# Performance work log

Measured on AMD Instinct MI355X. Metric: run time of the kernel, lower is better.

The kernel has to match this reference:

```python
import jax, jax.numpy as jnp
import numpy as np
from math import sqrt

B, S, E, H = 4, 2048, 1024, 16
D = E // H  # per-head dim = 64


def setup_inputs() -> dict:
    key = jax.random.key(0)
    ks = jax.random.split(key, 11)
    f = lambda k, shape, scale=1.0: jax.random.normal(k, shape, dtype=jnp.float32) * scale
    return {
        "Q": f(ks[0], (B, S, E)),
        "K": f(ks[1], (B, S, E)),
        "V": f(ks[2], (B, S, E)),
        "Wq": f(ks[3], (E, E), 1.0 / sqrt(E)),
        "bq": f(ks[4], (E,), 0.02),
        "Wk": f(ks[5], (E, E), 1.0 / sqrt(E)),
        "bk": f(ks[6], (E,), 0.02),
        "Wv": f(ks[7], (E, E), 1.0 / sqrt(E)),
        "bv": f(ks[8], (E,), 0.02),
        "Wo": f(ks[9], (E, E), 1.0 / sqrt(E)),
        "bo": f(ks[10], (E,), 0.02),
    }


def reference(Q, K, V, Wq, bq, Wk, bk, Wv, bv, Wo, bo):
    # Linear projections (torch Linear: x @ W.T + b)
    q = Q @ Wq.T + bq  # [B,S,E]
    k = K @ Wk.T + bk
    v = V @ Wv.T + bv
    # torch.chunk along last dim into H heads == reshape [B,S,H,D]
    q = q.reshape(B, S, H, D)
    k = k.reshape(B, S, H, D)
    v = v.reshape(B, S, H, D)
    scale = 1.0 / sqrt(D)
    # batched-over-heads scaled dot-product attention
    scores = jnp.einsum("bqhd,bkhd->bhqk", q, k) * scale  # [B,H,S,S]
    attn = jax.nn.softmax(scores, axis=-1)
    out = jnp.einsum("bhqk,bkhd->bqhd", attn, v).reshape(B, S, E)
    # dropout p=0.0 -> identity
    return out @ Wo.T + bo
```

## Files before the change

kernel.cpp:

```cpp
#include <hip/hip_runtime.h>
#include <hip/hip_bf16.h>

#define B_SZ   4
#define S_LEN  2048
#define E_DIM  1024
#define H_NUM  16
#define D_DIM  64
#define M_ROWS (B_SZ * S_LEN)
#define QK_SCALE 0.1803368801111204f

typedef __attribute__((ext_vector_type(8))) __bf16 bf16x8;
typedef __attribute__((ext_vector_type(4))) float  f32x4;

__device__ __forceinline__ bf16x8 load8(const void* p) {
    return __builtin_bit_cast(bf16x8, *reinterpret_cast<const uint4*>(p));
}

#if defined(__has_builtin)
#if __has_builtin(__builtin_amdgcn_exp2f)
#define EXP2F(x) __builtin_amdgcn_exp2f(x)
#endif
#if __has_builtin(__builtin_amdgcn_global_load_lds)
#define HAVE_GLL 1
#endif
#endif
#ifndef EXP2F
#define EXP2F(x) exp2f(x)
#endif

__device__ __forceinline__ void stage16(const __hip_bfloat16* g, __hip_bfloat16* lbase, int lane) {
#ifdef HAVE_GLL
    __builtin_amdgcn_global_load_lds((const __attribute__((address_space(1))) unsigned int*)g,
                                     (__attribute__((address_space(3))) unsigned int*)lbase,
                                     16, 0, 0);
#else
    reinterpret_cast<uint4*>(lbase)[lane] = *reinterpret_cast<const uint4*>(g);
#endif
}

#define N8A (1 << 20)
#define N8W (1 << 17)
#define N8TOT (3 * N8A + 4 * N8W)

struct CvtArgs {
    const float* s[7];
    __hip_bfloat16* d[7];
};

__global__ __launch_bounds__(256) void cvt_all(CvtArgs a)
{
    const int i = blockIdx.x * 256 + threadIdx.x;
    if (i >= N8TOT) return;
    int seg, off;
    if (i < 3 * N8A) { seg = i >> 20;              off = i & (N8A - 1); }
    else             { const int j = i - 3 * N8A;
                       seg = 3 + (j >> 17);        off = j & (N8W - 1); }
    const float* s = a.s[seg];
    __hip_bfloat16* d = a.d[seg];
    const float4 x = reinterpret_cast<const float4*>(s)[off * 2];
    const float4 y = reinterpret_cast<const float4*>(s)[off * 2 + 1];
    __hip_bfloat16 o[8];
    o[0] = __float2bfloat16(x.x); o[1] = __float2bfloat16(x.y);
    o[2] = __float2bfloat16(x.z); o[3] = __float2bfloat16(x.w);
    o[4] = __float2bfloat16(y.x); o[5] = __float2bfloat16(y.y);
    o[6] = __float2bfloat16(y.z); o[7] = __float2bfloat16(y.w);
    reinterpret_cast<uint4*>(d)[off] = *reinterpret_cast<uint4*>(o);
}

__global__ __launch_bounds__(256) void cvt_f32_bf16(const float* __restrict__ s,
                                                    __hip_bfloat16* __restrict__ d,
                                                    int n8)
{
    const int i = blockIdx.x * 256 + threadIdx.x;
    if (i >= n8) return;
    const float4 a = reinterpret_cast<const float4*>(s)[i * 2];
    const float4 b = reinterpret_cast<const float4*>(s)[i * 2 + 1];
    __hip_bfloat16 o[8];
    o[0] = __float2bfloat16(a.x); o[1] = __float2bfloat16(a.y);
    o[2] = __float2bfloat16(a.z); o[3] = __float2bfloat16(a.w);
    o[4] = __float2bfloat16(b.x); o[5] = __float2bfloat16(b.y);
    o[6] = __float2bfloat16(b.z); o[7] = __float2bfloat16(b.w);
    reinterpret_cast<uint4*>(d)[i] = *reinterpret_cast<uint4*>(o);
}

struct GemmArgs {
    const __hip_bfloat16* A[3];
    const __hip_bfloat16* W[3];
    const float* bias[3];
    void* C[3];
    float scale[3];
    int mode[3];
};

__global__ __launch_bounds__(512, 4) void gemm_bt(GemmArgs g)
{
    __shared__ __attribute__((aligned(16))) char lds_raw[3 * 24576];

    const int tid = threadIdx.x;
    const int wid = tid >> 6, lane = tid & 63;
    const int quad = lane >> 4, l16 = lane & 15;
    const int wm = wid >> 2, wn = wid & 3;

    const int seg = blockIdx.x >> 8;
    int bid = blockIdx.x & 255;
    bid = (bid & 7) * 32 + (bid >> 3);
    const int bm = bid >> 2, bn = bid & 3;
    const int row0 = bm * 128, col0 = bn * 256;

    const __hip_bfloat16* A = g.A[seg];
    const __hip_bfloat16* W = g.W[seg];

    const int s_line = tid >> 3, s_gr = tid & 7;
    const int glin  = s_gr ^ (s_line & 7);
    const int s_row = (s_line << 1) + (glin >> 2);
    const int s_ks  = glin & 3;
    const __hip_bfloat16* gA = A + (size_t)(row0 + s_row) * E_DIM + s_ks * 8;
    const __hip_bfloat16* gB = W + (size_t)(col0 + s_row) * E_DIM + s_ks * 8;
    const int stA = wid << 10;

    const int rg   = (((l16 & 1) << 2) | quad) ^ ((l16 >> 1) & 7);
    const int aoff = (wm * 32 + (l16 >> 1)) * 128 + rg * 16;
    const int boff = (wn * 32 + (l16 >> 1)) * 128 + rg * 16;

    f32x4 acc[4][4];
    const f32x4 zero = {0.f, 0.f, 0.f, 0.f};
#pragma unroll
    for (int i = 0; i < 4; i++)
#pragma unroll
        for (int j = 0; j < 4; j++) acc[i][j] = zero;

    auto stage_t = [&](int t) {
        char* b = lds_raw + (t % 3) * 24576;
        const int ko = t * 32;
        stage16(gA + ko, (__hip_bfloat16*)(b + stA), lane);
        stage16(gB + ko, (__hip_bfloat16*)(b + 8192 + stA), lane);
        stage16(gB + (size_t)128 * E_DIM + ko, (__hip_bfloat16*)(b + 16384 + stA), lane);
    };

    auto body = [&](int t, bool stg) {
        __builtin_amdgcn_s_barrier();
        __builtin_amdgcn_sched_barrier(0);
        if (stg) stage_t(t + 2);
        const char* ab = lds_raw + (t % 3) * 24576;
        bf16x8 af[4], bf[4];
#pragma unroll
        for (int i = 0; i < 4; i++) af[i] = load8(ab + aoff + i * 1024);
#pragma unroll
        for (int j = 0; j < 4; j++) bf[j] = load8(ab + 8192 + boff + j * 1024);
        __builtin_amdgcn_s_setprio(1);
#pragma unroll
        for (int i = 0; i < 4; i++)
#pragma unroll
            for (int j = 0; j < 4; j++)
                acc[i][j] = __builtin_amdgcn_mfma_f32_16x16x32_bf16(af[i], bf[j], acc[i][j], 0, 0, 0);
        __builtin_amdgcn_s_setprio(0);
        __builtin_amdgcn_sched_barrier(0);
    };

    const int NT = E_DIM / 32;
    stage_t(0); stage_t(1);
    for (int t = 0; t < NT - 2; ++t) {
        asm volatile("s_waitcnt vmcnt(3)" ::: "memory");
        body(t, true);
    }
    asm volatile("s_waitcnt vmcnt(3)" ::: "memory"); body(NT - 2, false);
    asm volatile("s_waitcnt vmcnt(0)" ::: "memory"); body(NT - 1, false);

    const int   mode  = g.mode[seg];
    const float scale = g.scale[seg];
    const float* bias = g.bias[seg];
    void* Cout        = g.C[seg];
#pragma unroll
    for (int j = 0; j < 4; j++) {
        const int col = col0 + wn * 64 + j * 16 + l16;
        const float bv = bias[col];
#pragma unroll
        for (int i = 0; i < 4; i++) {
            const int row = row0 + wm * 64 + i * 16 + quad * 4;
            if (mode == 3) {
                __attribute__((aligned(8))) __hip_bfloat16 o[4];
#pragma unroll
                for (int r = 0; r < 4; r++) o[r] = __float2bfloat16((acc[i][j][r] + bv) * scale);
                const int b_ = row >> 11, s_ = row & 2047, h_ = col >> 6, d_ = col & 63;
                *reinterpret_cast<uint2*>((__hip_bfloat16*)Cout +
                    (((size_t)(b_ * H_NUM + h_)) << 17) + (d_ << 11) + s_) =
                    *reinterpret_cast<uint2*>(o);
            } else {
#pragma unroll
                for (int r = 0; r < 4; r++) {
                    const float v = (acc[i][j][r] + bv) * scale;
                    const int rr = row + r;
                    if (mode == 0) {
                        ((__hip_bfloat16*)Cout)[(size_t)rr * E_DIM + col] = __float2bfloat16(v);
                    } else if (mode == 1) {
                        ((float*)Cout)[(size_t)rr * E_DIM + col] = v;
                    } else {
                        const int b_ = rr >> 11, s_ = rr & 2047, h_ = col >> 6, d_ = col & 63;
                        ((__hip_bfloat16*)Cout)[(((size_t)(b_ * H_NUM + h_)) << 17) + (s_ << 6) + d_] =
                            __float2bfloat16(v);
                    }
                }
            }
        }
    }
}

__global__ __launch_bounds__(256) void attn(const __hip_bfloat16* __restrict__ Qt,
                                            const __hip_bfloat16* __restrict__ Kt,
                                            const __hip_bfloat16* __restrict__ Vt,
                                            __hip_bfloat16* __restrict__ Op)
{
    __shared__ __hip_bfloat16 Pls[4][64][40];
    __shared__ __attribute__((aligned(16))) __hip_bfloat16 Kls[2][32 * 64];
    __shared__ __attribute__((aligned(16))) __hip_bfloat16 Vls[2][64 * 32];

    const int x = blockIdx.x;
    const int xcd = x & 7, idx = x >> 3;
    const int bh     = xcd * 8 + (idx & 7);
    const int qchunk = idx >> 3;
    const int tid = threadIdx.x;
    const int wave = tid >> 6, lane = tid & 63;
    const int quad = lane >> 4, l16 = lane & 15;
    const int qrow0 = qchunk * 256 + wave * 64;

    const __hip_bfloat16* qb = Qt + ((size_t)bh << 17);
    const __hip_bfloat16* kb = Kt + ((size_t)bh << 17);
    const __hip_bfloat16* vb = Vt + ((size_t)bh << 17);
    __hip_bfloat16* pw = &Pls[wave][0][0];

    const int skey = tid >> 3, sgk = (tid & 7) ^ (skey & 7);
    const __hip_bfloat16* kSrc = kb + (skey << 6) + (sgk << 3);
    const int sd = tid >> 2, sgv = (tid & 3) ^ ((sd >> 1) & 3);
    const __hip_bfloat16* vSrc = vb + ((size_t)sd << 11) + (sgv << 3);
    const int stW = wave << 10;

    const int ksw = l16 & 7, vsw = (l16 >> 1) & 3;

    bf16x8 qf[4][2];
#pragma unroll
    for (int qt = 0; qt < 4; qt++) {
        qf[qt][0] = load8(qb + ((qrow0 + qt * 16 + l16) << 6) + quad * 8);
        qf[qt][1] = load8(qb + ((qrow0 + qt * 16 + l16) << 6) + 32 + quad * 8);
    }

    const f32x4 zero = {0.f, 0.f, 0.f, 0.f};
    f32x4 o_acc[4][4];
#pragma unroll
    for (int qt = 0; qt < 4; qt++)
#pragma unroll
        for (int dj = 0; dj < 4; dj++) o_acc[qt][dj] = zero;
    float lsum[4] = {0.f, 0.f, 0.f, 0.f};

    auto stageKV = [&](int kv, int b) {
        stage16(kSrc + (kv << 6), (__hip_bfloat16*)((char*)&Kls[b][0] + stW), lane);
        stage16(vSrc + kv,        (__hip_bfloat16*)((char*)&Vls[b][0] + stW), lane);
    };

    auto compute = [&](int b) {
        const char* Kbuf = (const char*)&Kls[b][0];
        const char* Vbuf = (const char*)&Vls[b][0];
#pragma unroll
        for (int t = 0; t < 2; t++) {
            const bf16x8 ka = load8(Kbuf + ((t * 16 + l16) << 7) + ((quad ^ ksw) << 4));
            const bf16x8 kc = load8(Kbuf + ((t * 16 + l16) << 7) + (((quad + 4) ^ ksw) << 4));
#pragma unroll
            for (int qt = 0; qt < 4; qt++) {
                f32x4 st = __builtin_amdgcn_mfma_f32_16x16x32_bf16(ka, qf[qt][0], zero, 0, 0, 0);
                st       = __builtin_amdgcn_mfma_f32_16x16x32_bf16(kc, qf[qt][1], st, 0, 0, 0);
                const float p0 = EXP2F(st[0]), p1 = EXP2F(st[1]);
                const float p2 = EXP2F(st[2]), p3 = EXP2F(st[3]);
                lsum[qt] += (p0 + p1) + (p2 + p3);
                const unsigned u0 = (unsigned)__bfloat16_as_ushort(__float2bfloat16(p0));
                const unsigned u1 = (unsigned)__bfloat16_as_ushort(__float2bfloat16(p1));
                const unsigned u2 = (unsigned)__bfloat16_as_ushort(__float2bfloat16(p2));
                const unsigned u3 = (unsigned)__bfloat16_as_ushort(__float2bfloat16(p3));
                uint2 w;
                w.x = (u1 << 16) | u0;
                w.y = (u3 << 16) | u2;
                *reinterpret_cast<uint2*>(&pw[(qt * 16 + l16) * 40 + t * 16 + quad * 4]) = w;
            }
        }
        bf16x8 vf[4];
#pragma unroll
        for (int dj = 0; dj < 4; dj++)
            vf[dj] = load8(Vbuf + ((dj * 16 + l16) << 6) + ((quad ^ vsw) << 4));
        __builtin_amdgcn_s_setprio(1);
#pragma unroll
        for (int qt = 0; qt < 4; qt++) {
            const bf16x8 pa = load8(&pw[(qt * 16 + l16) * 40 + quad * 8]);
#pragma unroll
            for (int dj = 0; dj < 4; dj++)
                o_acc[qt][dj] = __builtin_amdgcn_mfma_f32_16x16x32_bf16(pa, vf[dj], o_acc[qt][dj], 0, 0, 0);
        }
        __builtin_amdgcn_s_setprio(0);
    };

    stageKV(0, 0);
    int cur = 0;
    for (int kv0 = 0; kv0 < S_LEN; kv0 += 32) {
        __syncthreads();
        if (kv0 + 32 < S_LEN) stageKV(kv0 + 32, cur ^ 1);
        compute(cur);
        cur ^= 1;
    }

    const int b_ = bh >> 4, h_ = bh & 15;
#pragma unroll
    for (int qt = 0; qt < 4; qt++) {
        float l = lsum[qt];
        l += __shfl_xor(l, 16, 64);
        l += __shfl_xor(l, 32, 64);
#pragma unroll
        for (int r = 0; r < 4; r++) {
            const float lr = __shfl(l, quad * 4 + r, 64);
            const float inv = 1.f / lr;
            const size_t ro = ((size_t)b_ * S_LEN + (qrow0 + qt * 16 + quad * 4 + r)) * E_DIM + h_ * D_DIM;
#pragma unroll
            for (int dj = 0; dj < 4; dj++)
                Op[ro + dj * 16 + l16] = __float2bfloat16(o_acc[qt][dj][r] * inv);
        }
    }
}

extern "C" void kernel_launch(void* const* d_in, const int* in_sizes, int n_in,
                              void* d_out, int out_size, void* d_ws, size_t ws_size,
                              hipStream_t stream)
{
    const float* Qf  = (const float*)d_in[0];
    const float* Kf  = (const float*)d_in[1];
    const float* Vf  = (const float*)d_in[2];
    const float* Wqf = (const float*)d_in[3];
    const float* bqf = (const float*)d_in[4];
    const float* Wkf = (const float*)d_in[5];
    const float* bkf = (const float*)d_in[6];
    const float* Wvf = (const float*)d_in[7];
    const float* bvf = (const float*)d_in[8];
    const float* Wof = (const float*)d_in[9];
    const float* bof = (const float*)d_in[10];

    const size_t n_act = (size_t)M_ROWS * E_DIM;
    const size_t n_w   = (size_t)E_DIM * E_DIM;

    const dim3 blk(256), gblk(512), ablk(256);
    const int cg_act = (int)(n_act / 8 / 256);
    const int cg_w   = (int)(n_w / 8 / 256);

    const size_t need_fast = (6 * n_act + 4 * n_w) * sizeof(__hip_bfloat16);

    if (ws_size >= need_fast) {
        __hip_bfloat16* Xq = (__hip_bfloat16*)d_ws;
        __hip_bfloat16* Xk = Xq + n_act;
        __hip_bfloat16* Xv = Xk + n_act;
        __hip_bfloat16* Wb = Xv + n_act;
        __hip_bfloat16* Qt = Wb + 4 * n_w;
        __hip_bfloat16* Kt = Qt + n_act;
        __hip_bfloat16* Vt = Kt + n_act;

        CvtArgs ca;
        ca.s[0] = Qf;  ca.s[1] = Kf;  ca.s[2] = Vf;
        ca.s[3] = Wqf; ca.s[4] = Wkf; ca.s[5] = Wvf; ca.s[6] = Wof;
        ca.d[0] = Xq;  ca.d[1] = Xk;  ca.d[2] = Xv;
        ca.d[3] = Wb;  ca.d[4] = Wb + n_w; ca.d[5] = Wb + 2 * n_w; ca.d[6] = Wb + 3 * n_w;
        cvt_all<<<dim3(N8TOT / 256), blk, 0, stream>>>(ca);

        GemmArgs qkv;
        qkv.A[0] = Xq;  qkv.A[1] = Xk;  qkv.A[2] = Xv;
        qkv.W[0] = Wb;  qkv.W[1] = Wb + n_w;  qkv.W[2] = Wb + 2*n_w;
        qkv.bias[0] = bqf;  qkv.bias[1] = bkf;  qkv.bias[2] = bvf;
        qkv.C[0] = Qt;  qkv.C[1] = Kt;  qkv.C[2] = Vt;
        qkv.scale[0] = QK_SCALE;  qkv.scale[1] = 1.0f;  qkv.scale[2] = 1.0f;
        qkv.mode[0] = 2;  qkv.mode[1] = 2;  qkv.mode[2] = 3;
        gemm_bt<<<dim3(768), gblk, 0, stream>>>(qkv);

        attn<<<dim3(512), ablk, 0, stream>>>(Qt, Kt, Vt, Xq);

        GemmArgs og;
        og.A[0] = Xq;  og.A[1] = Xq;  og.A[2] = Xq;
        og.W[0] = Wb + 3*n_w;  og.W[1] = og.W[0];  og.W[2] = og.W[0];
        og.bias[0] = bof;  og.bias[1] = bof;  og.bias[2] = bof;
        og.C[0] = d_out;  og.C[1] = d_out;  og.C[2] = d_out;
        og.scale[0] = 1.0f;  og.scale[1] = 1.0f;  og.scale[2] = 1.0f;
        og.mode[0] = 1;  og.mode[1] = 1;  og.mode[2] = 1;
        gemm_bt<<<dim3(256), gblk, 0, stream>>>(og);
    } else {
        __hip_bfloat16* X  = (__hip_bfloat16*)d_ws;
        __hip_bfloat16* Wb = X + n_act;
        __hip_bfloat16* Qt = Wb + n_w;
        __hip_bfloat16* Kt = Qt + n_act;
        __hip_bfloat16* Vt = Kt + n_act;

        auto one = [&](const float* Af, const float* Wf, const float* bf_,
                       void* C, float sc, int md) {
            cvt_f32_bf16<<<cg_act, blk, 0, stream>>>(Af, X, (int)(n_act / 8));
            cvt_f32_bf16<<<cg_w,   blk, 0, stream>>>(Wf, Wb, (int)(n_w / 8));
            GemmArgs a;
            a.A[0] = X; a.A[1] = X; a.A[2] = X;
            a.W[0] = Wb; a.W[1] = Wb; a.W[2] = Wb;
            a.bias[0] = bf_; a.bias[1] = bf_; a.bias[2] = bf_;
            a.C[0] = C; a.C[1] = C; a.C[2] = C;
            a.scale[0] = sc; a.scale[1] = sc; a.scale[2] = sc;
            a.mode[0] = md; a.mode[1] = md; a.mode[2] = md;
            gemm_bt<<<dim3(256), gblk, 0, stream>>>(a);
        };
        one(Qf, Wqf, bqf, Qt, QK_SCALE, 2);
        one(Kf, Wkf, bkf, Kt, 1.0f, 2);
        one(Vf, Wvf, bvf, Vt, 1.0f, 3);
        attn<<<dim3(512), ablk, 0, stream>>>(Qt, Kt, Vt, X);
        cvt_f32_bf16<<<cg_w, blk, 0, stream>>>(Wof, Wb, (int)(n_w / 8));
        GemmArgs og;
        og.A[0] = X; og.A[1] = X; og.A[2] = X;
        og.W[0] = Wb; og.W[1] = Wb; og.W[2] = Wb;
        og.bias[0] = bof; og.bias[1] = bof; og.bias[2] = bof;
        og.C[0] = d_out; og.C[1] = d_out; og.C[2] = d_out;
        og.scale[0] = 1.0f; og.scale[1] = 1.0f; og.scale[2] = 1.0f;
        og.mode[0] = 1; og.mode[1] = 1; og.mode[2] = 1;
        gemm_bt<<<dim3(256), gblk, 0, stream>>>(og);
    }
}
```

Measured before the change: 331.4 us.

## Enlarge GEMM tile to 256x256 with 4-phase pipeline; double attention block size

The projection GEMM moves from 128x256 tiles with K-step 32 and triple buffering to 256x256 tiles with K-step 64. Each iteration is split into four MFMA phases interleaved with staging of the next tile into a double-buffered 128KB LDS. This raises arithmetic intensity per byte loaded, at the cost of occupancy (launch bounds 2), far fewer blocks (384 and 128), and more accumulator registers. The attention kernel now uses 512 threads covering 512 query rows per block, with K and V staged by separate halves of the block, so each staged K/V tile is shared by more queries.

```diff
diff --git a/kernel.cpp b/kernel.cpp
--- a/kernel.cpp
+++ b/kernel.cpp
@@ -90,81 +90,120 @@
     void* C[3];
     float scale[3];
     int mode[3];
+    int nper;
 };
 
-__global__ __launch_bounds__(512, 4) void gemm_bt(GemmArgs g)
+__global__ __launch_bounds__(512, 2) void gemm_bt(GemmArgs g)
 {
-    __shared__ __attribute__((aligned(16))) char lds_raw[3 * 24576];
+    __shared__ __attribute__((aligned(16))) char lds[2][65536];
 
     const int tid = threadIdx.x;
     const int wid = tid >> 6, lane = tid & 63;
     const int quad = lane >> 4, l16 = lane & 15;
     const int wm = wid >> 2, wn = wid & 3;
 
-    const int seg = blockIdx.x >> 8;
-    int bid = blockIdx.x & 255;
-    bid = (bid & 7) * 32 + (bid >> 3);
+    const int cpx = gridDim.x >> 3;
+    const int id  = (blockIdx.x & 7) * cpx + (blockIdx.x >> 3);
+    const int seg = id / g.nper;
+    const int bid = id % g.nper;
     const int bm = bid >> 2, bn = bid & 3;
-    const int row0 = bm * 128, col0 = bn * 256;
+    const int row0 = bm * 256, col0 = bn * 256;
 
     const __hip_bfloat16* A = g.A[seg];
     const __hip_bfloat16* W = g.W[seg];
 
-    const int s_line = tid >> 3, s_gr = tid & 7;
-    const int glin  = s_gr ^ (s_line & 7);
-    const int s_row = (s_line << 1) + (glin >> 2);
-    const int s_ks  = glin & 3;
-    const __hip_bfloat16* gA = A + (size_t)(row0 + s_row) * E_DIM + s_ks * 8;
-    const __hip_bfloat16* gB = W + (size_t)(col0 + s_row) * E_DIM + s_ks * 8;
-    const int stA = wid << 10;
-
-    const int rg   = (((l16 & 1) << 2) | quad) ^ ((l16 >> 1) & 7);
-    const int aoff = (wm * 32 + (l16 >> 1)) * 128 + rg * 16;
-    const int boff = (wn * 32 + (l16 >> 1)) * 128 + rg * 16;
-
-    f32x4 acc[4][4];
+    const int srow = tid >> 3;
+    const int sgk  = (tid & 7) ^ (srow & 7);
+    const __hip_bfloat16* aSrc = A + (size_t)(row0 + srow) * E_DIM + sgk * 8;
+    const __hip_bfloat16* bSrc = W + (size_t)(col0 + srow) * E_DIM + sgk * 8;
+    const int stW = wid << 10;
+
+    const int abase = (wm * 128 + l16) * 128;
+    const int bbase = 32768 + (wn * 64 + l16) * 128;
+    const int sl0 = ((quad)     ^ (l16 & 7)) << 4;
+    const int sl1 = ((quad | 4) ^ (l16 & 7)) << 4;
+
+    f32x4 acc[8][4];
     const f32x4 zero = {0.f, 0.f, 0.f, 0.f};
 #pragma unroll
-    for (int i = 0; i < 4; i++)
+    for (int i = 0; i < 8; i++)
 #pragma unroll
         for (int j = 0; j < 4; j++) acc[i][j] = zero;
 
-    auto stage_t = [&](int t) {
-        char* b = lds_raw + (t % 3) * 24576;
-        const int ko = t * 32;
-        stage16(gA + ko, (__hip_bfloat16*)(b + stA), lane);
-        stage16(gB + ko, (__hip_bfloat16*)(b + 8192 + stA), lane);
-        stage16(gB + (size_t)128 * E_DIM + ko, (__hip_bfloat16*)(b + 16384 + stA), lane);
+    auto stage = [&](int t, int c) {
+        char* d = lds[t & 1];
+        stage16(aSrc + (size_t)c * 64 * E_DIM + t * 64,
+                (__hip_bfloat16*)(d + c * 8192 + stW), lane);
+        stage16(bSrc + (size_t)c * 64 * E_DIM + t * 64,
+                (__hip_bfloat16*)(d + 32768 + c * 8192 + stW), lane);
     };
 
-    auto body = [&](int t, bool stg) {
+#define PHASE_TAIL()                                             \
+    __builtin_amdgcn_s_barrier();                                \
+    asm volatile("s_waitcnt lgkmcnt(0)" ::: "memory");           \
+    __builtin_amdgcn_sched_barrier(0);                           \
+    __builtin_amdgcn_s_setprio(1);
+
+#define PHASE_END()                                              \
+    __builtin_amdgcn_s_setprio(0);                               \
+    __builtin_amdgcn_s_barrier();
+
+    const int NT = E_DIM / 64;
+    stage(0, 0); stage(0, 1); stage(0, 2); stage(0, 3);
+    for (int t = 0; t < NT; ++t) {
+        const bool pf = (t + 1 < NT);
+        const char* base = lds[t & 1];
+        if (pf) { stage(t + 1, 0); stage(t + 1, 1);
+                  asm volatile("s_waitcnt vmcnt(4)" ::: "memory"); }
+        else    { asm volatile("s_waitcnt vmcnt(0)" ::: "memory"); }
         __builtin_amdgcn_s_barrier();
-        __builtin_amdgcn_sched_barrier(0);
-        if (stg) stage_t(t + 2);
-        const char* ab = lds_raw + (t % 3) * 24576;
+
         bf16x8 af[4], bf[4];
 #pragma unroll
-        for (int i = 0; i < 4; i++) af[i] = load8(ab + aoff + i * 1024);
-#pragma unroll
-        for (int j = 0; j < 4; j++) bf[j] = load8(ab + 8192 + boff + j * 1024);
-        __builtin_amdgcn_s_setprio(1);
+        for (int j = 0; j < 4; j++) bf[j] = load8(base + bbase + j * 2048 + sl0);
+#pragma unroll
+        for (int i = 0; i < 4; i++) af[i] = load8(base + abase + i * 2048 + sl0);
+        PHASE_TAIL()
 #pragma unroll
         for (int i = 0; i < 4; i++)
 #pragma unroll
             for (int j = 0; j < 4; j++)
                 acc[i][j] = __builtin_amdgcn_mfma_f32_16x16x32_bf16(af[i], bf[j], acc[i][j], 0, 0, 0);
-        __builtin_amdgcn_s_setprio(0);
-        __builtin_amdgcn_sched_barrier(0);
-    };
-
-    const int NT = E_DIM / 32;
-    stage_t(0); stage_t(1);
-    for (int t = 0; t < NT - 2; ++t) {
-        asm volatile("s_waitcnt vmcnt(3)" ::: "memory");
-        body(t, true);
-    }
-    asm volatile("s_waitcnt vmcnt(3)" ::: "memory"); body(NT - 2, false);
-    asm volatile("s_waitcnt vmcnt(0)" ::: "memory"); body(NT - 1, false);
+        PHASE_END()
+#pragma unroll
+        for (int i = 0; i < 4; i++) af[i] = load8(base + abase + (i + 4) * 2048 + sl0);
+        if (pf) stage(t + 1, 2);
+        PHASE_TAIL()
+#pragma unroll
+        for (int i = 0; i < 4; i++)
+#pragma unroll
+            for (int j = 0; j < 4; j++)
+                acc[i + 4][j] = __builtin_amdgcn_mfma_f32_16x16x32_bf16(af[i], bf[j], acc[i + 4][j], 0, 0, 0);
+        PHASE_END()
+#pragma unroll
+        for (int j = 0; j < 4; j++) bf[j] = load8(base + bbase + j * 2048 + sl1);
+#pragma unroll
+        for (int i = 0; i < 4; i++) af[i] = load8(base + abase + i * 2048 + sl1);
+        if (pf) stage(t + 1, 3);
+        PHASE_TAIL()
+#pragma unroll
+        for (int i = 0; i < 4; i++)
+#pragma unroll
+            for (int j = 0; j < 4; j++)
+                acc[i][j] = __builtin_amdgcn_mfma_f32_16x16x32_bf16(af[i], bf[j], acc[i][j], 0, 0, 0);
+        PHASE_END()
+#pragma unroll
+        for (int i = 0; i < 4; i++) af[i] = load8(base + abase + (i + 4) * 2048 + sl1);
+        PHASE_TAIL()
+#pragma unroll
+        for (int i = 0; i < 4; i++)
+#pragma unroll
+            for (int j = 0; j < 4; j++)
+                acc[i + 4][j] = __builtin_amdgcn_mfma_f32_16x16x32_bf16(af[i], bf[j], acc[i + 4][j], 0, 0, 0);
+        PHASE_END()
+    }
+#undef PHASE_TAIL
+#undef PHASE_END
 
     const int   mode  = g.mode[seg];
     const float scale = g.scale[seg];
@@ -175,8 +214,8 @@
         const int col = col0 + wn * 64 + j * 16 + l16;
         const float bv = bias[col];
 #pragma unroll
-        for (int i = 0; i < 4; i++) {
-            const int row = row0 + wm * 64 + i * 16 + quad * 4;
+        for (int i = 0; i < 8; i++) {
+            const int row = row0 + wm * 128 + i * 16 + quad * 4;
             if (mode == 3) {
                 __attribute__((aligned(8))) __hip_bfloat16 o[4];
 #pragma unroll
@@ -205,34 +244,34 @@
     }
 }
 
-__global__ __launch_bounds__(256) void attn(const __hip_bfloat16* __restrict__ Qt,
+__global__ __launch_bounds__(512) void attn(const __hip_bfloat16* __restrict__ Qt,
                                             const __hip_bfloat16* __restrict__ Kt,
                                             const __hip_bfloat16* __restrict__ Vt,
                                             __hip_bfloat16* __restrict__ Op)
 {
-    __shared__ __hip_bfloat16 Pls[4][64][40];
+    __shared__ __hip_bfloat16 Pls[8][64][40];
     __shared__ __attribute__((aligned(16))) __hip_bfloat16 Kls[2][32 * 64];
     __shared__ __attribute__((aligned(16))) __hip_bfloat16 Vls[2][64 * 32];
 
     const int x = blockIdx.x;
-    const int xcd = x & 7, idx = x >> 3;
-    const int bh     = xcd * 8 + (idx & 7);
-    const int qchunk = idx >> 3;
+    const int bh     = (x & 7) * 8 + ((x >> 3) & 7);
+    const int qchunk = x >> 6;
     const int tid = threadIdx.x;
     const int wave = tid >> 6, lane = tid & 63;
     const int quad = lane >> 4, l16 = lane & 15;
-    const int qrow0 = qchunk * 256 + wave * 64;
+    const int qrow0 = qchunk * 512 + wave * 64;
 
     const __hip_bfloat16* qb = Qt + ((size_t)bh << 17);
     const __hip_bfloat16* kb = Kt + ((size_t)bh << 17);
     const __hip_bfloat16* vb = Vt + ((size_t)bh << 17);
     __hip_bfloat16* pw = &Pls[wave][0][0];
 
-    const int skey = tid >> 3, sgk = (tid & 7) ^ (skey & 7);
+    const int rt = tid & 255;
+    const int skey = rt >> 3, sgk = (rt & 7) ^ (skey & 7);
     const __hip_bfloat16* kSrc = kb + (skey << 6) + (sgk << 3);
-    const int sd = tid >> 2, sgv = (tid & 3) ^ ((sd >> 1) & 3);
+    const int sd = rt >> 2, sgv = (rt & 3) ^ ((sd >> 1) & 3);
     const __hip_bfloat16* vSrc = vb + ((size_t)sd << 11) + (sgv << 3);
-    const int stW = wave << 10;
+    const int stW = (wave & 3) << 10;
 
     const int ksw = l16 & 7, vsw = (l16 >> 1) & 3;
 
@@ -252,8 +291,10 @@
     float lsum[4] = {0.f, 0.f, 0.f, 0.f};
 
     auto stageKV = [&](int kv, int b) {
-        stage16(kSrc + (kv << 6), (__hip_bfloat16*)((char*)&Kls[b][0] + stW), lane);
-        stage16(vSrc + kv,        (__hip_bfloat16*)((char*)&Vls[b][0] + stW), lane);
+        if (tid < 256)
+            stage16(kSrc + (kv << 6), (__hip_bfloat16*)((char*)&Kls[b][0] + stW), lane);
+        else
+            stage16(vSrc + kv,        (__hip_bfloat16*)((char*)&Vls[b][0] + stW), lane);
     };
 
     auto compute = [&](int b) {
@@ -341,7 +382,7 @@
     const size_t n_act = (size_t)M_ROWS * E_DIM;
     const size_t n_w   = (size_t)E_DIM * E_DIM;
 
-    const dim3 blk(256), gblk(512), ablk(256);
+    const dim3 blk(256), gblk(512), ablk(512);
     const int cg_act = (int)(n_act / 8 / 256);
     const int cg_w   = (int)(n_w / 8 / 256);
 
@@ -370,9 +411,10 @@
         qkv.C[0] = Qt;  qkv.C[1] = Kt;  qkv.C[2] = Vt;
         qkv.scale[0] = QK_SCALE;  qkv.scale[1] = 1.0f;  qkv.scale[2] = 1.0f;
         qkv.mode[0] = 2;  qkv.mode[1] = 2;  qkv.mode[2] = 3;
-        gemm_bt<<<dim3(768), gblk, 0, stream>>>(qkv);
-
-        attn<<<dim3(512), ablk, 0, stream>>>(Qt, Kt, Vt, Xq);
+        qkv.nper = 128;
+        gemm_bt<<<dim3(384), gblk, 0, stream>>>(qkv);
+
+        attn<<<dim3(256), ablk, 0, stream>>>(Qt, Kt, Vt, Xq);
 
         GemmArgs og;
         og.A[0] = Xq;  og.A[1] = Xq;  og.A[2] = Xq;
@@ -381,7 +423,8 @@
         og.C[0] = d_out;  og.C[1] = d_out;  og.C[2] = d_out;
         og.scale[0] = 1.0f;  og.scale[1] = 1.0f;  og.scale[2] = 1.0f;
         og.mode[0] = 1;  og.mode[1] = 1;  og.mode[2] = 1;
-        gemm_bt<<<dim3(256), gblk, 0, stream>>>(og);
+        og.nper = 128;
+        gemm_bt<<<dim3(128), gblk, 0, stream>>>(og);
     } else {
         __hip_bfloat16* X  = (__hip_bfloat16*)d_ws;
         __hip_bfloat16* Wb = X + n_act;
@@ -400,12 +443,13 @@
             a.C[0] = C; a.C[1] = C; a.C[2] = C;
             a.scale[0] = sc; a.scale[1] = sc; a.scale[2] = sc;
             a.mode[0] = md; a.mode[1] = md; a.mode[2] = md;
-            gemm_bt<<<dim3(256), gblk, 0, stream>>>(a);
+            a.nper = 128;
+            gemm_bt<<<dim3(128), gblk, 0, stream>>>(a);
         };
         one(Qf, Wqf, bqf, Qt, QK_SCALE, 2);
         one(Kf, Wkf, bkf, Kt, 1.0f, 2);
         one(Vf, Wvf, bvf, Vt, 1.0f, 3);
-        attn<<<dim3(512), ablk, 0, stream>>>(Qt, Kt, Vt, X);
+        attn<<<dim3(256), ablk, 0, stream>>>(Qt, Kt, Vt, X);
         cvt_f32_bf16<<<cg_w, blk, 0, stream>>>(Wof, Wb, (int)(n_w / 8));
         GemmArgs og;
         og.A[0] = X; og.A[1] = X; og.A[2] = X;
@@ -414,6 +458,7 @@
         og.C[0] = d_out; og.C[1] = d_out; og.C[2] = d_out;
         og.scale[0] = 1.0f; og.scale[1] = 1.0f; og.scale[2] = 1.0f;
         og.mode[0] = 1; og.mode[1] = 1; og.mode[2] = 1;
-        gemm_bt<<<dim3(256), gblk, 0, stream>>>(og);
-    }
-}
+        og.nper = 128;
+        gemm_bt<<<dim3(128), gblk, 0, stream>>>(og);
+    }
+}
```

Result: slower. 370.1 us (+11.7%).

## Fuse fp32-to-bf16 activation conversion into QKV projection GEMM

Applied to the files above, without the earlier changes.

Removes the separate conversion pass over the Q, K and V activations. The QKV GEMM now loads fp32 A tiles directly, converts them to bf16 in registers and writes them to LDS, while weights are still pre-converted by a smaller kernel. This avoids writing and rereading the bf16 activation copies, but A staging now goes through registers instead of direct global-to-LDS loads, which can add latency and register pressure in the main loop.

```diff
diff --git a/kernel.cpp b/kernel.cpp
--- a/kernel.cpp
+++ b/kernel.cpp
@@ -40,21 +40,17 @@
 
 #define N8A (1 << 20)
 #define N8W (1 << 17)
-#define N8TOT (3 * N8A + 4 * N8W)
-
-struct CvtArgs {
-    const float* s[7];
-    __hip_bfloat16* d[7];
+
+struct CvtWArgs {
+    const float* s[4];
+    __hip_bfloat16* d[4];
 };
 
-__global__ __launch_bounds__(256) void cvt_all(CvtArgs a)
+__global__ __launch_bounds__(256) void cvt_w(CvtWArgs a)
 {
     const int i = blockIdx.x * 256 + threadIdx.x;
-    if (i >= N8TOT) return;
-    int seg, off;
-    if (i < 3 * N8A) { seg = i >> 20;              off = i & (N8A - 1); }
-    else             { const int j = i - 3 * N8A;
-                       seg = 3 + (j >> 17);        off = j & (N8W - 1); }
+    if (i >= 4 * N8W) return;
+    const int seg = i >> 17, off = i & (N8W - 1);
     const float* s = a.s[seg];
     __hip_bfloat16* d = a.d[seg];
     const float4 x = reinterpret_cast<const float4*>(s)[off * 2];
@@ -92,7 +88,152 @@
     int mode[3];
 };
 
-__global__ __launch_bounds__(512, 4) void gemm_bt(GemmArgs g)
+struct GemmQArgs {
+    const float* Af[3];
+    const __hip_bfloat16* W[3];
+    const float* bias[3];
+    void* C[3];
+    float scale[3];
+    int mode[3];
+};
+
+__global__ __launch_bounds__(512, 4) void gemm_qkvf(GemmQArgs g)
+{
+    __shared__ __attribute__((aligned(16))) char lds_raw[3 * 24576];
+
+    const int tid = threadIdx.x;
+    const int wid = tid >> 6, lane = tid & 63;
+    const int quad = lane >> 4, l16 = lane & 15;
+    const int wm = wid >> 2, wn = wid & 3;
+
+    const int seg = blockIdx.x >> 8;
+    int bid = blockIdx.x & 255;
+    bid = (bid & 7) * 32 + (bid >> 3);
+    const int bm = bid >> 2, bn = bid & 3;
+    const int row0 = bm * 128, col0 = bn * 256;
+
+    const float* Af = g.Af[seg];
+    const __hip_bfloat16* W = g.W[seg];
+
+    const int s_line = tid >> 3, s_gr = tid & 7;
+    const int glin  = s_gr ^ (s_line & 7);
+    const int s_row = (s_line << 1) + (glin >> 2);
+    const int s_ks  = glin & 3;
+    const float* gAf = Af + (size_t)(row0 + s_row) * E_DIM + s_ks * 8;
+    const __hip_bfloat16* gB = W + (size_t)(col0 + s_row) * E_DIM + s_ks * 8;
+    const int stA = wid << 10;
+
+    const int rg   = (((l16 & 1) << 2) | quad) ^ ((l16 >> 1) & 7);
+    const int aoff = (wm * 32 + (l16 >> 1)) * 128 + rg * 16;
+    const int boff = (wn * 32 + (l16 >> 1)) * 128 + rg * 16;
+
+    f32x4 acc[4][4];
+    const f32x4 zero = {0.f, 0.f, 0.f, 0.f};
+#pragma unroll
+    for (int i = 0; i < 4; i++)
+#pragma unroll
+        for (int j = 0; j < 4; j++) acc[i][j] = zero;
+
+    auto stageB = [&](int t) {
+        char* b = lds_raw + (t % 3) * 24576;
+        const int ko = t * 32;
+        stage16(gB + ko, (__hip_bfloat16*)(b + 8192 + stA), lane);
+        stage16(gB + (size_t)128 * E_DIM + ko, (__hip_bfloat16*)(b + 16384 + stA), lane);
+    };
+
+    auto writeA = [&](int t, float4 u, float4 v) {
+        char* b = lds_raw + (t % 3) * 24576;
+        __attribute__((aligned(16))) __hip_bfloat16 o[8];
+        o[0] = __float2bfloat16(u.x); o[1] = __float2bfloat16(u.y);
+        o[2] = __float2bfloat16(u.z); o[3] = __float2bfloat16(u.w);
+        o[4] = __float2bfloat16(v.x); o[5] = __float2bfloat16(v.y);
+        o[6] = __float2bfloat16(v.z); o[7] = __float2bfloat16(v.w);
+        *reinterpret_cast<uint4*>(b + tid * 16) = *reinterpret_cast<uint4*>(o);
+    };
+
+    auto inner = [&](int t, bool stg) {
+        __builtin_amdgcn_s_barrier();
+        __builtin_amdgcn_sched_barrier(0);
+        float4 u{}, v{};
+        if (stg) {
+            u = *reinterpret_cast<const float4*>(gAf + (t + 2) * 32);
+            v = *reinterpret_cast<const float4*>(gAf + (t + 2) * 32 + 4);
+            stageB(t + 2);
+        }
+        const char* ab = lds_raw + (t % 3) * 24576;
+        bf16x8 af[4], bf[4];
+#pragma unroll
+        for (int i = 0; i < 4; i++) af[i] = load8(ab + aoff + i * 1024);
+#pragma unroll
+        for (int j = 0; j < 4; j++) bf[j] = load8(ab + 8192 + boff + j * 1024);
+        __builtin_amdgcn_s_setprio(1);
+#pragma unroll
+        for (int i = 0; i < 4; i++)
+#pragma unroll
+            for (int j = 0; j < 4; j++)
+                acc[i][j] = __builtin_amdgcn_mfma_f32_16x16x32_bf16(af[i], bf[j], acc[i][j], 0, 0, 0);
+        __builtin_amdgcn_s_setprio(0);
+        if (stg) writeA(t + 2, u, v);
+        asm volatile("s_waitcnt lgkmcnt(0)" ::: "memory");
+        __builtin_amdgcn_sched_barrier(0);
+    };
+
+    const float4 p00 = *reinterpret_cast<const float4*>(gAf + 0);
+    const float4 p01 = *reinterpret_cast<const float4*>(gAf + 4);
+    const float4 p10 = *reinterpret_cast<const float4*>(gAf + 32);
+    const float4 p11 = *reinterpret_cast<const float4*>(gAf + 36);
+    stageB(0); stageB(1);
+    writeA(0, p00, p01); writeA(1, p10, p11);
+    asm volatile("s_waitcnt lgkmcnt(0)" ::: "memory");
+
+    const int NT = E_DIM / 32;
+    for (int t = 0; t < NT - 2; ++t) {
+        asm volatile("s_waitcnt vmcnt(2)" ::: "memory");
+        inner(t, true);
+    }
+    asm volatile("s_waitcnt vmcnt(2)" ::: "memory"); inner(NT - 2, false);
+    asm volatile("s_waitcnt vmcnt(0)" ::: "memory"); inner(NT - 1, false);
+
+    const int   mode  = g.mode[seg];
+    const float scale = g.scale[seg];
+    const float* bias = g.bias[seg];
+    void* Cout        = g.C[seg];
+#pragma unroll
+    for (int j = 0; j < 4; j++) {
+        const int col = col0 + wn * 64 + j * 16 + l16;
+        const float bv = bias[col];
+#pragma unroll
+        for (int i = 0; i < 4; i++) {
+            const int row = row0 + wm * 64 + i * 16 + quad * 4;
+            if (mode == 3) {
+                __attribute__((aligned(8))) __hip_bfloat16 o[4];
+#pragma unroll
+                for (int r = 0; r < 4; r++) o[r] = __float2bfloat16((acc[i][j][r] + bv) * scale);
+                const int b_ = row >> 11, s_ = row & 2047, h_ = col >> 6, d_ = col & 63;
+                *reinterpret_cast<uint2*>((__hip_bfloat16*)Cout +
+                    (((size_t)(b_ * H_NUM + h_)) << 17) + (d_ << 11) + s_) =
+                    *reinterpret_cast<uint2*>(o);
+            } else {
+#pragma unroll
+                for (int r = 0; r < 4; r++) {
+                    const float v = (acc[i][j][r] + bv) * scale;
+                    const int rr = row + r;
+                    if (mode == 0) {
+                        ((__hip_bfloat16*)Cout)[(size_t)rr * E_DIM + col] = __float2bfloat16(v);
+                    } else if (mode == 1) {
+                        ((float*)Cout)[(size_t)rr * E_DIM + col] = v;
+                    } else {
+                        const int b_ = rr >> 11, s_ = rr & 2047, h_ = col >> 6, d_ = col & 63;
+                        ((__hip_bfloat16*)Cout)[(((size_t)(b_ * H_NUM + h_)) << 17) + (s_ << 6) + d_] =
+                            __float2bfloat16(v);
+                    }
+                }
+            }
+        }
+    }
+}
+
+__global__ __launch_bounds__(512, 4) void gemm_og(GemmArgs g)
 {
     __shared__ __attribute__((aligned(16))) char lds_raw[3 * 24576];
 
@@ -345,43 +486,39 @@
     const int cg_act = (int)(n_act / 8 / 256);
     const int cg_w   = (int)(n_w / 8 / 256);
 
-    const size_t need_fast = (6 * n_act + 4 * n_w) * sizeof(__hip_bfloat16);
+    const size_t need_fast = (4 * n_act + 4 * n_w) * sizeof(__hip_bfloat16);
 
     if (ws_size >= need_fast) {
-        __hip_bfloat16* Xq = (__hip_bfloat16*)d_ws;
-        __hip_bfloat16* Xk = Xq + n_act;
-        __hip_bfloat16* Xv = Xk + n_act;
-        __hip_bfloat16* Wb = Xv + n_act;
+        __hip_bfloat16* Wb = (__hip_bfloat16*)d_ws;
         __hip_bfloat16* Qt = Wb + 4 * n_w;
         __hip_bfloat16* Kt = Qt + n_act;
         __hip_bfloat16* Vt = Kt + n_act;
-
-        CvtArgs ca;
-        ca.s[0] = Qf;  ca.s[1] = Kf;  ca.s[2] = Vf;
-        ca.s[3] = Wqf; ca.s[4] = Wkf; ca.s[5] = Wvf; ca.s[6] = Wof;
-        ca.d[0] = Xq;  ca.d[1] = Xk;  ca.d[2] = Xv;
-        ca.d[3] = Wb;  ca.d[4] = Wb + n_w; ca.d[5] = Wb + 2 * n_w; ca.d[6] = Wb + 3 * n_w;
-        cvt_all<<<dim3(N8TOT / 256), blk, 0, stream>>>(ca);
-
-        GemmArgs qkv;
-        qkv.A[0] = Xq;  qkv.A[1] = Xk;  qkv.A[2] = Xv;
+        __hip_bfloat16* Xo = Vt + n_act;
+
+        CvtWArgs cw;
+        cw.s[0] = Wqf; cw.s[1] = Wkf; cw.s[2] = Wvf; cw.s[3] = Wof;
+        cw.d[0] = Wb;  cw.d[1] = Wb + n_w; cw.d[2] = Wb + 2 * n_w; cw.d[3] = Wb + 3 * n_w;
+        cvt_w<<<dim3(4 * N8W / 256), blk, 0, stream>>>(cw);
+
+        GemmQArgs qkv;
+        qkv.Af[0] = Qf;  qkv.Af[1] = Kf;  qkv.Af[2] = Vf;
         qkv.W[0] = Wb;  qkv.W[1] = Wb + n_w;  qkv.W[2] = Wb + 2*n_w;
         qkv.bias[0] = bqf;  qkv.bias[1] = bkf;  qkv.bias[2] = bvf;
         qkv.C[0] = Qt;  qkv.C[1] = Kt;  qkv.C[2] = Vt;
         qkv.scale[0] = QK_SCALE;  qkv.scale[1] = 1.0f;  qkv.scale[2] = 1.0f;
         qkv.mode[0] = 2;  qkv.mode[1] = 2;  qkv.mode[2] = 3;
-        gemm_bt<<<dim3(768), gblk, 0, stream>>>(qkv);
-
-        attn<<<dim3(512), ablk, 0, stream>>>(Qt, Kt, Vt, Xq);
+        gemm_qkvf<<<dim3(768), gblk, 0, stream>>>(qkv);
+
+        attn<<<dim3(512), ablk, 0, stream>>>(Qt, Kt, Vt, Xo);
 
         GemmArgs og;
-        og.A[0] = Xq;  og.A[1] = Xq;  og.A[2] = Xq;
+        og.A[0] = Xo;  og.A[1] = Xo;  og.A[2] = Xo;
         og.W[0] = Wb + 3*n_w;  og.W[1] = og.W[0];  og.W[2] = og.W[0];
         og.bias[0] = bof;  og.bias[1] = bof;  og.bias[2] = bof;
         og.C[0] = d_out;  og.C[1] = d_out;  og.C[2] = d_out;
         og.scale[0] = 1.0f;  og.scale[1] = 1.0f;  og.scale[2] = 1.0f;
         og.mode[0] = 1;  og.mode[1] = 1;  og.mode[2] = 1;
-        gemm_bt<<<dim3(256), gblk, 0, stream>>>(og);
+        gemm_og<<<dim3(256), gblk, 0, stream>>>(og);
     } else {
         __hip_bfloat16* X  = (__hip_bfloat16*)d_ws;
         __hip_bfloat16* Wb = X + n_act;
@@ -400,7 +537,7 @@
             a.C[0] = C; a.C[1] = C; a.C[2] = C;
             a.scale[0] = sc; a.scale[1] = sc; a.scale[2] = sc;
             a.mode[0] = md; a.mode[1] = md; a.mode[2] = md;
-            gemm_bt<<<dim3(256), gblk, 0, stream>>>(a);
+            gemm_og<<<dim3(256), gblk, 0, stream>>>(a);
         };
         one(Qf, Wqf, bqf, Qt, QK_SCALE, 2);
         one(Kf, Wkf, bkf, Kt, 1.0f, 2);
@@ -414,6 +551,6 @@
         og.C[0] = d_out; og.C[1] = d_out; og.C[2] = d_out;
         og.scale[0] = 1.0f; og.scale[1] = 1.0f; og.scale[2] = 1.0f;
         og.mode[0] = 1; og.mode[1] = 1; og.mode[2] = 1;
-        gemm_bt<<<dim3(256), gblk, 0, stream>>>(og);
-    }
-}
+        gemm_og<<<dim3(256), gblk, 0, stream>>>(og);
+    }
+}
```

New measurement: 378.9 us. +14.3%, slower.
